# Optimization experiments

Measured on AMD Instinct MI355X. Metric: run time of the kernel, lower is better.

Reference implementation:

```python
import jax, jax.numpy as jnp
import numpy as np

B, N, E, D = 4, 50000, 800000, 64


def setup_inputs() -> dict:
    key = jax.random.key(0)
    k_h, k_e, k_w1, k_w2 = jax.random.split(key, 4)
    s = 1.0 / np.sqrt(D)  # glorot-ish scale for 64x64 linear weights
    return {
        "t": jnp.zeros((1,), jnp.float32),
        "h": jax.random.normal(k_h, (B, N, D), jnp.float32),
        "edge_index": jax.random.randint(k_e, (2, E), 0, N, jnp.int32),
        "W1": jax.random.normal(k_w1, (D, D), jnp.float32) * s,
        "b1": jnp.zeros((D,), jnp.float32),
        "W2": jax.random.normal(k_w2, (D, D), jnp.float32) * s,
        "b2": jnp.zeros((D,), jnp.float32),
    }


def _gcn(x, row, col, norm, W, b, n_nodes):
    # x: (B, N, D). PyG GCNConv: linear (no bias) -> normalized gather/scatter -> +bias
    xw = jnp.einsum("bnd,de->bne", x, W)
    msg = xw[:, row, :] * norm[None, :, None]          # (B, E+N, D)
    agg = jax.vmap(lambda m: jax.ops.segment_sum(m, col, num_segments=n_nodes))(msg)
    return agg + b


def reference(t, h, edge_index, W1, b1, W2, b2):
    n_nodes = h.shape[1]
    loop = jnp.arange(n_nodes, dtype=edge_index.dtype)
    # add self-loops (PyG GCNConv default)
    row = jnp.concatenate([edge_index[0], loop])  # source nodes
    col = jnp.concatenate([edge_index[1], loop])  # target nodes
    # symmetric normalization D^{-1/2} (A+I) D^{-1/2}; degree counted on targets
    deg = jax.ops.segment_sum(jnp.ones_like(row, dtype=h.dtype), col, num_segments=n_nodes)
    dis = jnp.where(deg > 0, jax.lax.rsqrt(deg), 0.0)
    norm = dis[row] * dis[col]
    h = jnp.tanh(_gcn(h, row, col, norm, W1, b1, n_nodes))
    h = jnp.tanh(_gcn(h, row, col, norm, W2, b2, n_nodes))
    return h
```

## Files before the change

kernel.cpp:

```cpp
#include <hip/hip_runtime.h>
#include <math.h>

#define B_ 4
#define N_ 50000
#define E_ 800000
#define D_ 64
#define M_ (B_*N_)

typedef _Float16 h4 __attribute__((ext_vector_type(4)));
typedef _Float16 h8 __attribute__((ext_vector_type(8)));
typedef float    f4 __attribute__((ext_vector_type(4)));

__global__ __launch_bounds__(256) void k_count(const int4* __restrict__ col4, int* __restrict__ cnt) {
  int e = blockIdx.x * 256 + threadIdx.x;
  if (e < E_ / 4) {
    int4 c = col4[e];
    atomicAdd(&cnt[c.x], 1);
    atomicAdd(&cnt[c.y], 1);
    atomicAdd(&cnt[c.z], 1);
    atomicAdd(&cnt[c.w], 1);
  }
}

__global__ __launch_bounds__(1024) void k_scan_a(const int* __restrict__ cnt, int* __restrict__ part,
                                                 float* __restrict__ dis) {
  __shared__ int sd[1024];
  int i = blockIdx.x * 1024 + threadIdx.x;
  int v = (i < N_) ? cnt[i] : 0;
  if (i < N_) dis[i] = 1.0f / sqrtf((float)(v + 1));
  sd[threadIdx.x] = v;
  __syncthreads();
  for (int s = 512; s > 0; s >>= 1) {
    if (threadIdx.x < s) sd[threadIdx.x] += sd[threadIdx.x + s];
    __syncthreads();
  }
  if (threadIdx.x == 0) part[blockIdx.x] = sd[0];
}

__global__ __launch_bounds__(1024) void k_scan_c(const int* __restrict__ cnt, const int* __restrict__ part,
                                                 int* __restrict__ off, int* __restrict__ cur) {
  __shared__ int sd[1024];
  __shared__ int base_s;
  int i = blockIdx.x * 1024 + threadIdx.x;
  int v = (i < N_) ? cnt[i] : 0;
  if (threadIdx.x == 0) {
    int b = 0;
    for (int j = 0; j < (int)blockIdx.x; j++) b += part[j];
    base_s = b;
  }
  sd[threadIdx.x] = v;
  __syncthreads();
  for (int s = 1; s < 1024; s <<= 1) {
    int t = (threadIdx.x >= s) ? sd[threadIdx.x - s] : 0;
    __syncthreads();
    sd[threadIdx.x] += t;
    __syncthreads();
  }
  int incl = sd[threadIdx.x];
  if (i < N_) { off[i] = base_s + incl - v; cur[i] = 0; }
  if (i == N_ - 1) off[N_] = base_s + incl;
}

__global__ __launch_bounds__(256) void k_fill(const int* __restrict__ row, const int* __restrict__ col,
                                              const int* __restrict__ off, int* __restrict__ cur,
                                              const float* __restrict__ dis,
                                              int2* __restrict__ em) {
  int e = blockIdx.x * 256 + threadIdx.x;
  if (e < E_) {
    int c = col[e], r = row[e];
    int p = off[c] + atomicAdd(&cur[c], 1);
    float w = dis[r] * dis[c];
    em[p] = make_int2(r, __float_as_int(w));
  }
}

__global__ __launch_bounds__(256) void k_wfrag(const float* __restrict__ W1, const float* __restrict__ W2,
                                               h8* __restrict__ Wf1, h8* __restrict__ Wf2) {
  int t0 = threadIdx.x;
  for (int w = 0; w < 2; w++) {
    const float* W = w ? W2 : W1;
    h8* Wf = w ? Wf2 : Wf1;
    for (int p = 0; p < 2; p++) {
      int fid = p * 256 + t0;
      int khalf = fid >> 8;
      int rem = fid & 255;
      int tt = rem >> 6;
      int lane = rem & 63;
      int kq = lane >> 4, m = lane & 15;
      h8 v;
#pragma unroll
      for (int j = 0; j < 8; j++) {
        int k = khalf * 32 + kq * 8 + j;
        v[j] = (_Float16)W[k * 64 + tt * 16 + m];
      }
      Wf[fid] = v;
    }
  }
}

template<int IN_F16>
__global__ __launch_bounds__(256) void k_linear(const void* __restrict__ Xv,
                                                const h8* __restrict__ Wf,
                                                _Float16* __restrict__ Y) {
  int wv = blockIdx.x * 4 + (threadIdx.x >> 6);
  int lane = threadIdx.x & 63;
  int m = lane & 15, kq = lane >> 4;
  size_t r0 = (size_t)wv * 16;
  h8 a0, a1;
  if constexpr (IN_F16) {
    const _Float16* xr = (const _Float16*)Xv + (r0 + m) * 64 + kq * 8;
    a0 = *(const h8*)(xr);
    a1 = *(const h8*)(xr + 32);
  } else {
    const float* xr = (const float*)Xv + (r0 + m) * 64 + kq * 8;
    f4 f0 = *(const f4*)(xr);
    f4 f1 = *(const f4*)(xr + 4);
    f4 f2 = *(const f4*)(xr + 32);
    f4 f3 = *(const f4*)(xr + 36);
#pragma unroll
    for (int j = 0; j < 4; j++) {
      a0[j] = (_Float16)f0[j]; a0[j + 4] = (_Float16)f1[j];
      a1[j] = (_Float16)f2[j]; a1[j + 4] = (_Float16)f3[j];
    }
  }
  f4 acc[4];
#pragma unroll
  for (int t = 0; t < 4; t++) {
    h8 b0 = Wf[t * 64 + lane];
    h8 b1 = Wf[256 + t * 64 + lane];
    f4 c = {0.f, 0.f, 0.f, 0.f};
    c = __builtin_amdgcn_mfma_f32_16x16x32_f16(a0, b0, c, 0, 0, 0);
    c = __builtin_amdgcn_mfma_f32_16x16x32_f16(a1, b1, c, 0, 0, 0);
    acc[t] = c;
  }
  int b  = (int)(r0 / N_);
  int n0 = (int)(r0 - (size_t)b * N_);
#pragma unroll
  for (int t = 0; t < 4; t++) {
#pragma unroll
    for (int r = 0; r < 4; r++) {
      int n = n0 + kq * 4 + r;
      Y[(size_t)n * 256 + b * 64 + t * 16 + m] = (_Float16)acc[t][r];
    }
  }
}

template<int OUT_F16>
__global__ __launch_bounds__(256, 5) void k_agg(const _Float16* __restrict__ xw,
                                                const int* __restrict__ off,
                                                const int2* __restrict__ em,
                                                const float* __restrict__ dis,
                                                const float* __restrict__ bias,
                                                void* __restrict__ outv) {
  int node = blockIdx.x * 4 + (threadIdx.x >> 6);
  int lane = threadIdx.x & 63;
  if (node >= N_) return;
  const h4* xp = (const h4*)xw;
  float d  = dis[node];
  float sw = d * d;
  f4 acc = __builtin_convertvector(xp[(size_t)node * 64 + lane], f4) * sw;
  int s = off[node], e = off[node + 1];
  while (s < e) {
    int i = s + lane;
    int2 mm = (i < e) ? em[i] : make_int2(0, 0);
    int er = mm.x;
    float wn = __int_as_float(mm.y);
    int c = e - s; if (c > 64) c = 64;
    for (int j = 0; j < c; j += 16) {
      int sn[16]; float w[16];
#pragma unroll
      for (int k = 0; k < 16; k++) {
        sn[k] = __shfl(er, j + k);
        w[k]  = __shfl(wn, j + k);
      }
      h4 v[16];
#pragma unroll
      for (int k = 0; k < 16; k++) v[k] = xp[(size_t)sn[k] * 64 + lane];
#pragma unroll
      for (int k = 0; k < 16; k++) acc += __builtin_convertvector(v[k], f4) * w[k];
    }
    s += 64;
  }
  int b  = lane >> 4;
  int d0 = (lane & 15) * 4;
  f4 bb = *(const f4*)(bias + d0);
  float r0 = tanhf(acc.x + bb.x);
  float r1 = tanhf(acc.y + bb.y);
  float r2 = tanhf(acc.z + bb.z);
  float r3 = tanhf(acc.w + bb.w);
  if constexpr (OUT_F16) {
    h4 o;
    o[0] = (_Float16)r0; o[1] = (_Float16)r1;
    o[2] = (_Float16)r2; o[3] = (_Float16)r3;
    *(h4*)((_Float16*)outv + ((size_t)b * N_ + node) * 64 + d0) = o;
  } else {
    f4 r = {r0, r1, r2, r3};
    *(f4*)((float*)outv + ((size_t)b * N_ + node) * 64 + d0) = r;
  }
}

extern "C" void kernel_launch(void* const* d_in, const int* in_sizes, int n_in,
                              void* d_out, int out_size, void* d_ws, size_t ws_size,
                              hipStream_t stream) {
  const float* h  = (const float*)d_in[1];
  const int*   ei = (const int*)d_in[2];
  const float* W1 = (const float*)d_in[3];
  const float* b1 = (const float*)d_in[4];
  const float* W2 = (const float*)d_in[5];
  const float* b2 = (const float*)d_in[6];
  float* out = (float*)d_out;
  const int* row = ei;
  const int* col = ei + E_;

  char* p = (char*)d_ws;
  _Float16* xw = (_Float16*)p; p += (size_t)M_ * D_ * sizeof(_Float16);
  int2* em  = (int2*)p;   p += (size_t)E_ * sizeof(int2);
  int*  cnt = (int*)p;    p += (size_t)N_ * sizeof(int);
  int*  off = (int*)p;    p += (size_t)(N_ + 4) * sizeof(int);
  int*  cur = (int*)p;    p += (size_t)N_ * sizeof(int);
  float* dis = (float*)p; p += (size_t)N_ * sizeof(float);
  int*  prt = (int*)p;    p += 64 * sizeof(int);
  h8*   Wf1 = (h8*)p;     p += 512 * sizeof(h8);
  h8*   Wf2 = (h8*)p;     p += 512 * sizeof(h8);
  _Float16* h1 = (_Float16*)d_out;

  hipMemsetAsync(cnt, 0, N_ * sizeof(int), stream);

  k_count<<<(E_ / 4 + 255) / 256, 256, 0, stream>>>((const int4*)col, cnt);
  int nscan = (N_ + 1023) / 1024;
  k_scan_a<<<nscan, 1024, 0, stream>>>(cnt, prt, dis);
  k_scan_c<<<nscan, 1024, 0, stream>>>(cnt, prt, off, cur);
  k_fill<<<(E_ + 255) / 256, 256, 0, stream>>>(row, col, off, cur, dis, em);
  k_wfrag<<<1, 256, 0, stream>>>(W1, W2, Wf1, Wf2);

  k_linear<0><<<M_ / 64, 256, 0, stream>>>(h, Wf1, xw);
  k_agg<1><<<N_ / 4, 256, 0, stream>>>(xw, off, em, dis, b1, h1);
  k_linear<1><<<M_ / 64, 256, 0, stream>>>(h1, Wf2, xw);
  k_agg<0><<<N_ / 4, 256, 0, stream>>>(xw, off, em, dis, b2, out);
}
```

Before: 337.5 us.

## Simplify aggregation loop with uniform edge loads and prescaled byte offsets

The aggregation kernel no longer loads edges cooperatively and broadcasts them with shuffles. Every lane now loads the same edge records, which are wave-uniform and likely become scalar loads, and gathers neighbor rows through byte offsets stored pre-shifted by 9 in the edge list. The self-loop weight is computed from the degree instead of reading dis, and blocks grow to 8 waves with the occupancy hint dropped. This removes shuffle overhead but gives up the 16-deep batching of gathers in favor of 8-deep unrolling, and the r<<9 offset relies on fitting in 32 bits.

Result: no change. 334.4 us (-0.9%).

```diff
diff --git a/kernel.cpp b/kernel.cpp
--- a/kernel.cpp
+++ b/kernel.cpp
@@ -70,7 +70,7 @@
     int c = col[e], r = row[e];
     int p = off[c] + atomicAdd(&cur[c], 1);
     float w = dis[r] * dis[c];
-    em[p] = make_int2(r, __float_as_int(w));
+    em[p] = make_int2(r << 9, __float_as_int(w));
   }
 }
 
@@ -146,41 +146,32 @@
 }
 
 template<int OUT_F16>
-__global__ __launch_bounds__(256, 5) void k_agg(const _Float16* __restrict__ xw,
-                                                const int* __restrict__ off,
-                                                const int2* __restrict__ em,
-                                                const float* __restrict__ dis,
-                                                const float* __restrict__ bias,
-                                                void* __restrict__ outv) {
-  int node = blockIdx.x * 4 + (threadIdx.x >> 6);
+__global__ __launch_bounds__(512) void k_agg(const _Float16* __restrict__ xw,
+                                             const int* __restrict__ off,
+                                             const int2* __restrict__ em,
+                                             const float* __restrict__ bias,
+                                             void* __restrict__ outv) {
+  int node = blockIdx.x * 8 + (threadIdx.x >> 6);
   int lane = threadIdx.x & 63;
-  if (node >= N_) return;
-  const h4* xp = (const h4*)xw;
-  float d  = dis[node];
-  float sw = d * d;
-  f4 acc = __builtin_convertvector(xp[(size_t)node * 64 + lane], f4) * sw;
-  int s = off[node], e = off[node + 1];
-  while (s < e) {
-    int i = s + lane;
-    int2 mm = (i < e) ? em[i] : make_int2(0, 0);
-    int er = mm.x;
-    float wn = __int_as_float(mm.y);
-    int c = e - s; if (c > 64) c = 64;
-    for (int j = 0; j < c; j += 16) {
-      int sn[16]; float w[16];
-#pragma unroll
-      for (int k = 0; k < 16; k++) {
-        sn[k] = __shfl(er, j + k);
-        w[k]  = __shfl(wn, j + k);
-      }
-      h4 v[16];
-#pragma unroll
-      for (int k = 0; k < 16; k++) v[k] = xp[(size_t)sn[k] * 64 + lane];
-#pragma unroll
-      for (int k = 0; k < 16; k++) acc += __builtin_convertvector(v[k], f4) * w[k];
-    }
-    s += 64;
-  }
+  const char* xb = (const char*)xw + (size_t)(lane * 8);
+  int s0 = __builtin_amdgcn_readfirstlane(off[node]);
+  int e0 = __builtin_amdgcn_readfirstlane(off[node + 1]);
+  float sw = 1.0f / (float)(e0 - s0 + 1);
+  h4 sv = *(const h4*)(xb + ((size_t)node << 9));
+  f4 acc = __builtin_convertvector(sv, f4) * sw;
+#define EDGE_(mm) do { \
+    h4 v_ = *(const h4*)(xb + (unsigned)(mm).x); \
+    acc += __builtin_convertvector(v_, f4) * __int_as_float((mm).y); \
+  } while (0)
+  int j = s0;
+  for (; j + 8 <= e0; j += 8) {
+    int2 m0 = em[j],     m1 = em[j + 1], m2 = em[j + 2], m3 = em[j + 3];
+    int2 m4 = em[j + 4], m5 = em[j + 5], m6 = em[j + 6], m7 = em[j + 7];
+    EDGE_(m0); EDGE_(m1); EDGE_(m2); EDGE_(m3);
+    EDGE_(m4); EDGE_(m5); EDGE_(m6); EDGE_(m7);
+  }
+  for (; j < e0; ++j) { int2 m = em[j]; EDGE_(m); }
+#undef EDGE_
   int b  = lane >> 4;
   int d0 = (lane & 15) * 4;
   f4 bb = *(const f4*)(bias + d0);
@@ -234,7 +225,7 @@
   k_wfrag<<<1, 256, 0, stream>>>(W1, W2, Wf1, Wf2);
 
   k_linear<0><<<M_ / 64, 256, 0, stream>>>(h, Wf1, xw);
-  k_agg<1><<<N_ / 4, 256, 0, stream>>>(xw, off, em, dis, b1, h1);
+  k_agg<1><<<N_ / 8, 512, 0, stream>>>(xw, off, em, b1, h1);
   k_linear<1><<<M_ / 64, 256, 0, stream>>>(h1, Wf2, xw);
-  k_agg<0><<<N_ / 4, 256, 0, stream>>>(xw, off, em, dis, b2, out);
-}
+  k_agg<0><<<N_ / 8, 512, 0, stream>>>(xw, off, em, b2, out);
+}
```
